# Kernel optimization log

Measured on AMD Instinct MI355X. Metric: run time of the kernel, lower is better.

The kernel has to match this reference:

```python
import jax, jax.numpy as jnp
import numpy as np

TAU = 0.01          # gumbel_softmax temperature
EPS = 1e-7          # tf.keras.backend.epsilon()
DEPTH = 5
N_NODES = 2 ** DEPTH - 1   # 31 internal nodes
N_LEAVES = 2 ** DEPTH      # 32 leaves


def _build_route():
    # route[l, node + dir*N_NODES] = 1 along the root-to-leaf path of leaf l
    # (same structure old_route_to_new_route produces for a perfect tree)
    route = np.zeros((N_LEAVES, 2 * N_NODES), dtype=np.float32)
    for l in range(N_LEAVES):
        node = 0
        for d in range(DEPTH):
            bit = (l >> (DEPTH - 1 - d)) & 1  # 0 = left, 1 = right
            route[l, node + bit * N_NODES] = 1.0
            node = 2 * node + 1 + bit
    return route


def setup_inputs() -> dict:
    B, F, T = 32768, 128, 100
    key = jax.random.key(0)
    k1, k2, k3, k4 = jax.random.split(key, 4)
    x = jax.random.normal(k1, (B, F), dtype=jnp.float32)
    kernel = jax.random.normal(k2, (T, F, N_NODES), dtype=jnp.float32) * 0.1
    bias = jax.random.normal(k3, (T, N_NODES), dtype=jnp.float32) * 0.1
    leaf = jax.random.normal(k4, (T, N_LEAVES), dtype=jnp.float32)
    route = jnp.asarray(_build_route())  # [L, 2N], shared tree topology
    return {"x": x, "kernel": kernel, "bias": bias, "leaf": leaf, "route": route}


def reference(x, kernel, bias, leaf, route):
    # NodeLayer: matmul(x, concat([K, -K], 1)) + concat([b, -b], 0)
    h = jnp.einsum("bf,tfn->btn", x, kernel) + bias          # [B, T, N]
    h2 = jnp.concatenate([h, -h], axis=-1)                   # [B, T, 2N]
    # activation1: log(clip(sigmoid(clip(h/tau, -32, 32)), eps, 1))
    a1 = jnp.log(jnp.clip(jax.nn.sigmoid(jnp.clip(h2 / TAU, -32.0, 32.0)), EPS, 1.0))
    # route aggregation: sum log-probs along each root->leaf path
    r = jnp.einsum("btm,lm->btl", a1, route)                 # [B, T, L]
    # activation2: exp(clip(., -32, 0)) -> leaf routing probabilities
    probs = jnp.exp(jnp.clip(r, -32.0, 0.0))
    # weight leaf values by route probabilities, sum over leaves and trees
    return jnp.einsum("btl,tl->b", probs, leaf)              # [B] raw GBM output
```

## Files before the change

### kernel.cpp

```cpp
#include <hip/hip_runtime.h>

typedef _Float16 f16x8  __attribute__((ext_vector_type(8)));
typedef float    f32x16 __attribute__((ext_vector_type(16)));
typedef float    f32x4  __attribute__((ext_vector_type(4)));

#define NTREES  100
#define WAVES   4
#define NCH     25
#define BM      64
#define KS      9
#define TSTRIDE (KS * 512)
#define NSCALE  (-144.269504088896f)

__device__ __forceinline__ int node_of_row(int sr, float& sg) {
  const int h   = (sr >> 2) & 1;
  const int reg = (sr & 3) + ((sr >> 3) << 2);
  sg = 1.0f;
  if (reg == 0) { if (h) sg = -1.0f; return 0; }
  if (reg == 1) return 1 + h;
  if (reg < 4)  return 1 + 2 * h + reg;
  if (reg < 8)  return 3 + 4 * h + reg;
  return 7 + 8 * h + reg;
}

__device__ __forceinline__ float exp2_fast(float v) {
#if __has_builtin(__builtin_amdgcn_exp2f)
  return __builtin_amdgcn_exp2f(v);
#else
  return exp2f(v);
#endif
}

__device__ __forceinline__ void nd_leaf(float ai, float Ll, float Lr,
                                        float& n, float& d) {
  const float emag = exp2_fast(-__builtin_fabsf(ai));
  const bool  sw   = ai > 0.0f;
  const float ta   = sw ? Ll : Lr;
  const float tb   = sw ? Lr : Ll;
  n = fmaf(emag, ta, tb);
  d = 1.0f + emag;
}
__device__ __forceinline__ void nd_int(float ai, float nl, float dl,
                                       float nr, float dr, float& n, float& d) {
  const float emag = exp2_fast(-__builtin_fabsf(ai));
  const float t0 = nl * dr, t1 = nr * dl;
  const bool  sw = ai > 0.0f;
  const float ta = sw ? t0 : t1;
  const float tb = sw ? t1 : t0;
  n = fmaf(emag, ta, tb);
  const float dd = dl * dr;
  d = fmaf(emag, dd, dd);
}

__device__ __forceinline__ float half_eval(const f32x16& a, const f32x4& L0,
                                           const f32x4& L1, const f32x4& L2,
                                           const f32x4& L3, float outAcc) {
  float n0,d0,n1,d1,n2,d2,n3,d3,n4,d4,n5,d5,n6,d6,n7,d7;
  nd_leaf(a[8],  L0[0], L0[1], n0, d0);
  nd_leaf(a[9],  L0[2], L0[3], n1, d1);
  nd_leaf(a[10], L1[0], L1[1], n2, d2);
  nd_leaf(a[11], L1[2], L1[3], n3, d3);
  nd_leaf(a[12], L2[0], L2[1], n4, d4);
  nd_leaf(a[13], L2[2], L2[3], n5, d5);
  nd_leaf(a[14], L3[0], L3[1], n6, d6);
  nd_leaf(a[15], L3[2], L3[3], n7, d7);
  float p0,q0,p1,q1,p2,q2,p3,q3;
  nd_int(a[4], n0, d0, n1, d1, p0, q0);
  nd_int(a[5], n2, d2, n3, d3, p1, q1);
  nd_int(a[6], n4, d4, n5, d5, p2, q2);
  nd_int(a[7], n6, d6, n7, d7, p3, q3);
  float u0,v0,u1,v1;
  nd_int(a[2], p0, q0, p1, q1, u0, v0);
  nd_int(a[3], p2, q2, p3, q3, u1, v1);
  float nf, df;
  nd_int(a[1], u0, v0, u1, v1, nf, df);
  const float emag0 = exp2_fast(-__builtin_fabsf(a[0]));
  const float dfin  = fmaf(emag0, df, df);
  const float nsc   = nf * emag0;
  const float nfin  = (a[0] > 0.0f) ? nsc : nf;
  return fmaf(nfin, __builtin_amdgcn_rcpf(dfin), outAcc);
}

__global__ void prep_b(const float* __restrict__ kern, const float* __restrict__ bias,
                       unsigned short* __restrict__ bws) {
  __shared__ float kt[128][32];
  __shared__ float bs[32];
  const int t = blockIdx.x, tid = threadIdx.x;
  const float* src = kern + (size_t)t * (128 * 31);
  for (int i = tid; i < 128 * 32; i += 512) {
    const int f = i >> 5, sr_ = i & 31;
    float sg; const int g = node_of_row(sr_, sg);
    kt[f][sr_] = src[f * 31 + g] * (NSCALE * sg);
  }
  if (tid < 32) {
    float sg; const int g = node_of_row(tid, sg);
    bs[tid] = bias[t * 31 + g] * (NSCALE * sg);
  }
  __syncthreads();
  unsigned short* dst = bws + (size_t)t * TSTRIDE;
  for (int s = tid; s < KS * 64; s += 512) {
    const int ks = s >> 6, lane = s & 63;
    const int row = lane & 31;
    const int k0 = ks * 16 + ((lane >> 5) << 3);
    f16x8 o;
    if (ks < 8) {
      #pragma unroll
      for (int j = 0; j < 8; ++j) o[j] = (_Float16)kt[k0 + j][row];
    } else {
      #pragma unroll
      for (int j = 0; j < 8; ++j) o[j] = (_Float16)0.0f;
      if (lane < 32) o[0] = (_Float16)bs[row];
    }
    *(f16x8*)(dst + s * 8) = o;
  }
}

__global__ __launch_bounds__(256, 3) void gbm_main(
    const float* __restrict__ x,
    const unsigned short* __restrict__ bws,
    const float* __restrict__ leaf,
    float* __restrict__ out)
{
  __shared__ __align__(16) unsigned char lds[2 * 8 * 64 * 16];
  float* red = (float*)lds;

  const int tid  = threadIdx.x;
  const int lane = tid & 63;
  const int w    = tid >> 6;
  const int rowbase = blockIdx.x * BM;

  #pragma unroll
  for (int T = 0; T < 2; ++T)
    for (int s = tid; s < 8 * 64; s += 256) {
      const int ks = s >> 6, l = s & 63;
      const int xrow = (l & 31) + T * 32;
      const int k0 = ks * 16 + ((l >> 5) << 3);
      const float* px = x + (size_t)(rowbase + xrow) * 128 + k0;
      float4 v0 = *(const float4*)px;
      float4 v1 = *(const float4*)(px + 4);
      f16x8 h8;
      h8[0] = (_Float16)v0.x; h8[1] = (_Float16)v0.y;
      h8[2] = (_Float16)v0.z; h8[3] = (_Float16)v0.w;
      h8[4] = (_Float16)v1.x; h8[5] = (_Float16)v1.y;
      h8[6] = (_Float16)v1.z; h8[7] = (_Float16)v1.w;
      *(f16x8*)(lds + T * 8192 + s * 16) = h8;
    }
  __syncthreads();

  f16x8 bx[2][8];
  #pragma unroll
  for (int T = 0; T < 2; ++T)
    #pragma unroll
    for (int ks = 0; ks < 8; ++ks)
      bx[T][ks] = *(const f16x8*)(lds + T * 8192 + (ks * 64 + lane) * 16);

  f16x8 bxb;
  #pragma unroll
  for (int j = 0; j < 8; ++j) bxb[j] = (_Float16)0.0f;
  if (lane < 32) bxb[0] = (_Float16)1.0f;

  f16x8 br[KS];
  {
    const unsigned short* bt = bws + (size_t)w * TSTRIDE;
    #pragma unroll
    for (int i = 0; i < KS; ++i)
      br[i] = *(const f16x8*)(bt + (size_t)i * 512 + lane * 8);
  }

  const int h = lane >> 5;
  float outAcc0 = 0.0f, outAcc1 = 0.0f;

  for (int c = 0; c < NCH; ++c) {
    const int tree = c * WAVES + w;

    const float* lp = leaf + (size_t)tree * 32 + (h << 4);
    f32x4 L0 = *(const f32x4*)lp;
    f32x4 L1 = *(const f32x4*)(lp + 4);
    f32x4 L2 = *(const f32x4*)(lp + 8);
    f32x4 L3 = *(const f32x4*)(lp + 12);

    f32x16 a0 = {};
    __builtin_amdgcn_s_setprio(1);
    #pragma unroll
    for (int ks = 0; ks < 8; ++ks)
      a0 = __builtin_amdgcn_mfma_f32_32x32x16_f16(br[ks], bx[0][ks], a0, 0, 0, 0);
    a0 = __builtin_amdgcn_mfma_f32_32x32x16_f16(br[8], bxb, a0, 0, 0, 0);
    __builtin_amdgcn_s_setprio(0);
    outAcc0 = half_eval(a0, L0, L1, L2, L3, outAcc0);

    f32x16 a1 = {};
    __builtin_amdgcn_s_setprio(1);
    #pragma unroll
    for (int ks = 0; ks < 8; ++ks)
      a1 = __builtin_amdgcn_mfma_f32_32x32x16_f16(br[ks], bx[1][ks], a1, 0, 0, 0);
    a1 = __builtin_amdgcn_mfma_f32_32x32x16_f16(br[8], bxb, a1, 0, 0, 0);
    __builtin_amdgcn_s_setprio(0);

    if (c + 1 < NCH) {
      const unsigned short* nb = bws + (size_t)((c + 1) * WAVES + w) * TSTRIDE;
      #pragma unroll
      for (int i = 0; i < KS; ++i)
        br[i] = *(const f16x8*)(nb + (size_t)i * 512 + lane * 8);
    }

    outAcc1 = half_eval(a1, L0, L1, L2, L3, outAcc1);
  }

  __syncthreads();
  red[tid] = outAcc0;
  red[256 + tid] = outAcc1;
  __syncthreads();
  if (tid < BM) {
    const int tile = tid >> 5, r = tid & 31;
    const float* rb = red + tile * 256 + r;
    float s = 0.0f;
    #pragma unroll
    for (int j = 0; j < 8; ++j)
      s += rb[((j >> 1) << 6) + ((j & 1) << 5)];
    out[rowbase + tid] = s;
  }
}

extern "C" void kernel_launch(void* const* d_in, const int* in_sizes, int n_in,
                              void* d_out, int out_size, void* d_ws, size_t ws_size,
                              hipStream_t stream) {
  const float* x    = (const float*)d_in[0];
  const float* kern = (const float*)d_in[1];
  const float* bias = (const float*)d_in[2];
  const float* leaf = (const float*)d_in[3];

  unsigned short* bws = (unsigned short*)d_ws;

  prep_b<<<NTREES, 512, 0, stream>>>(kern, bias, bws);
  gbm_main<<<32768 / BM, 256, 0, stream>>>(x, bws, leaf, (float*)d_out);
}
```

Measured before the change: 59.47 us.

## Split trees across two block groups with 8 waves and atomic output

Each row tile is now processed by two blocks, one per half of the trees (50 each), using 8 waves per block instead of 4. The per-wave register copy of the x operand is dropped: x fragments, with the bias column folded in as a ninth k-slice, are re-read from LDS before every MFMA. This frees registers and is meant to raise occupancy and parallelism. The costs are extra LDS traffic, uneven wave load (the last chunk has only 2 of 8 waves active), converting x twice, a memset launch, and atomicAdd for the final output.

```diff
diff --git a/kernel.cpp b/kernel.cpp
--- a/kernel.cpp
+++ b/kernel.cpp
@@ -5,8 +5,9 @@
 typedef float    f32x4  __attribute__((ext_vector_type(4)));
 
 #define NTREES  100
-#define WAVES   4
-#define NCH     25
+#define WAVES   8
+#define TPG     50
+#define NCH     7
 #define BM      64
 #define KS      9
 #define TSTRIDE (KS * 512)
@@ -115,109 +116,117 @@
   }
 }
 
-__global__ __launch_bounds__(256, 3) void gbm_main(
+__global__ __launch_bounds__(512, 4) void gbm_main(
     const float* __restrict__ x,
     const unsigned short* __restrict__ bws,
     const float* __restrict__ leaf,
     float* __restrict__ out)
 {
-  __shared__ __align__(16) unsigned char lds[2 * 8 * 64 * 16];
+  __shared__ __align__(16) unsigned char lds[2 * KS * 64 * 16];
   float* red = (float*)lds;
 
   const int tid  = threadIdx.x;
   const int lane = tid & 63;
   const int w    = tid >> 6;
+  const int g    = blockIdx.y;
   const int rowbase = blockIdx.x * BM;
 
   #pragma unroll
   for (int T = 0; T < 2; ++T)
-    for (int s = tid; s < 8 * 64; s += 256) {
+    for (int s = tid; s < KS * 64; s += 512) {
       const int ks = s >> 6, l = s & 63;
-      const int xrow = (l & 31) + T * 32;
-      const int k0 = ks * 16 + ((l >> 5) << 3);
-      const float* px = x + (size_t)(rowbase + xrow) * 128 + k0;
-      float4 v0 = *(const float4*)px;
-      float4 v1 = *(const float4*)(px + 4);
       f16x8 h8;
-      h8[0] = (_Float16)v0.x; h8[1] = (_Float16)v0.y;
-      h8[2] = (_Float16)v0.z; h8[3] = (_Float16)v0.w;
-      h8[4] = (_Float16)v1.x; h8[5] = (_Float16)v1.y;
-      h8[6] = (_Float16)v1.z; h8[7] = (_Float16)v1.w;
-      *(f16x8*)(lds + T * 8192 + s * 16) = h8;
+      if (ks < 8) {
+        const int xrow = (l & 31) + T * 32;
+        const int k0 = ks * 16 + ((l >> 5) << 3);
+        const float* px = x + (size_t)(rowbase + xrow) * 128 + k0;
+        float4 v0 = *(const float4*)px;
+        float4 v1 = *(const float4*)(px + 4);
+        h8[0] = (_Float16)v0.x; h8[1] = (_Float16)v0.y;
+        h8[2] = (_Float16)v0.z; h8[3] = (_Float16)v0.w;
+        h8[4] = (_Float16)v1.x; h8[5] = (_Float16)v1.y;
+        h8[6] = (_Float16)v1.z; h8[7] = (_Float16)v1.w;
+      } else {
+        #pragma unroll
+        for (int j = 0; j < 8; ++j) h8[j] = (_Float16)0.0f;
+        if (l < 32) h8[0] = (_Float16)1.0f;
+      }
+      *(f16x8*)(lds + T * (KS * 64 * 16) + s * 16) = h8;
     }
-  __syncthreads();
-
-  f16x8 bx[2][8];
-  #pragma unroll
-  for (int T = 0; T < 2; ++T)
-    #pragma unroll
-    for (int ks = 0; ks < 8; ++ks)
-      bx[T][ks] = *(const f16x8*)(lds + T * 8192 + (ks * 64 + lane) * 16);
-
-  f16x8 bxb;
-  #pragma unroll
-  for (int j = 0; j < 8; ++j) bxb[j] = (_Float16)0.0f;
-  if (lane < 32) bxb[0] = (_Float16)1.0f;
 
   f16x8 br[KS];
   {
-    const unsigned short* bt = bws + (size_t)w * TSTRIDE;
+    const unsigned short* bt = bws + (size_t)(g * TPG + w) * TSTRIDE;
     #pragma unroll
     for (int i = 0; i < KS; ++i)
       br[i] = *(const f16x8*)(bt + (size_t)i * 512 + lane * 8);
   }
 
+  __syncthreads();
+
   const int h = lane >> 5;
   float outAcc0 = 0.0f, outAcc1 = 0.0f;
 
   for (int c = 0; c < NCH; ++c) {
-    const int tree = c * WAVES + w;
-
-    const float* lp = leaf + (size_t)tree * 32 + (h << 4);
-    f32x4 L0 = *(const f32x4*)lp;
-    f32x4 L1 = *(const f32x4*)(lp + 4);
-    f32x4 L2 = *(const f32x4*)(lp + 8);
-    f32x4 L3 = *(const f32x4*)(lp + 12);
-
-    f32x16 a0 = {};
-    __builtin_amdgcn_s_setprio(1);
-    #pragma unroll
-    for (int ks = 0; ks < 8; ++ks)
-      a0 = __builtin_amdgcn_mfma_f32_32x32x16_f16(br[ks], bx[0][ks], a0, 0, 0, 0);
-    a0 = __builtin_amdgcn_mfma_f32_32x32x16_f16(br[8], bxb, a0, 0, 0, 0);
-    __builtin_amdgcn_s_setprio(0);
-    outAcc0 = half_eval(a0, L0, L1, L2, L3, outAcc0);
-
-    f32x16 a1 = {};
-    __builtin_amdgcn_s_setprio(1);
-    #pragma unroll
-    for (int ks = 0; ks < 8; ++ks)
-      a1 = __builtin_amdgcn_mfma_f32_32x32x16_f16(br[ks], bx[1][ks], a1, 0, 0, 0);
-    a1 = __builtin_amdgcn_mfma_f32_32x32x16_f16(br[8], bxb, a1, 0, 0, 0);
-    __builtin_amdgcn_s_setprio(0);
-
-    if (c + 1 < NCH) {
-      const unsigned short* nb = bws + (size_t)((c + 1) * WAVES + w) * TSTRIDE;
+    const int ti  = c * WAVES + w;
+    const bool act = ti < TPG;
+
+    if (act) {
+      const int tree = g * TPG + ti;
+      const float* lp = leaf + (size_t)tree * 32 + (h << 4);
+      f32x4 L0 = *(const f32x4*)lp;
+      f32x4 L1 = *(const f32x4*)(lp + 4);
+      f32x4 L2 = *(const f32x4*)(lp + 8);
+      f32x4 L3 = *(const f32x4*)(lp + 12);
+
+      f32x16 a0 = {};
+      __builtin_amdgcn_s_setprio(1);
+      #pragma unroll
+      for (int ks = 0; ks < KS; ++ks) {
+        f16x8 bx = *(const f16x8*)(lds + (ks * 64 + lane) * 16);
+        a0 = __builtin_amdgcn_mfma_f32_32x32x16_f16(br[ks], bx, a0, 0, 0, 0);
+      }
+      __builtin_amdgcn_s_setprio(0);
+      outAcc0 = half_eval(a0, L0, L1, L2, L3, outAcc0);
+
+      f32x16 a1 = {};
+      __builtin_amdgcn_s_setprio(1);
+      #pragma unroll
+      for (int ks = 0; ks < KS; ++ks) {
+        f16x8 bx = *(const f16x8*)(lds + KS * 64 * 16 + (ks * 64 + lane) * 16);
+        a1 = __builtin_amdgcn_mfma_f32_32x32x16_f16(br[ks], bx, a1, 0, 0, 0);
+      }
+      __builtin_amdgcn_s_setprio(0);
+
+      if ((c + 1) * WAVES + w < TPG) {
+        const unsigned short* nb =
+            bws + (size_t)(g * TPG + (c + 1) * WAVES + w) * TSTRIDE;
+        #pragma unroll
+        for (int i = 0; i < KS; ++i)
+          br[i] = *(const f16x8*)(nb + (size_t)i * 512 + lane * 8);
+      }
+
+      outAcc1 = half_eval(a1, L0, L1, L2, L3, outAcc1);
+    } else if ((c + 1) * WAVES + w < TPG) {
+      const unsigned short* nb =
+          bws + (size_t)(g * TPG + (c + 1) * WAVES + w) * TSTRIDE;
       #pragma unroll
       for (int i = 0; i < KS; ++i)
         br[i] = *(const f16x8*)(nb + (size_t)i * 512 + lane * 8);
     }
-
-    outAcc1 = half_eval(a1, L0, L1, L2, L3, outAcc1);
   }
 
   __syncthreads();
   red[tid] = outAcc0;
-  red[256 + tid] = outAcc1;
+  red[512 + tid] = outAcc1;
   __syncthreads();
   if (tid < BM) {
     const int tile = tid >> 5, r = tid & 31;
-    const float* rb = red + tile * 256 + r;
     float s = 0.0f;
     #pragma unroll
-    for (int j = 0; j < 8; ++j)
-      s += rb[((j >> 1) << 6) + ((j & 1) << 5)];
-    out[rowbase + tid] = s;
+    for (int j = 0; j < 16; ++j)
+      s += red[tile * 512 + j * 32 + r];
+    atomicAdd(out + rowbase + tid, s);
   }
 }
 
@@ -232,5 +241,6 @@
   unsigned short* bws = (unsigned short*)d_ws;
 
   prep_b<<<NTREES, 512, 0, stream>>>(kern, bias, bws);
-  gbm_main<<<32768 / BM, 256, 0, stream>>>(x, bws, leaf, (float*)d_out);
-}
+  hipMemsetAsync(d_out, 0, (size_t)out_size * sizeof(float), stream);
+  gbm_main<<<dim3(32768 / BM, 2), 512, 0, stream>>>(x, bws, leaf, (float*)d_out);
+}
```

Measured after the change: 55.83 us. 6.1% less time.
